# Kernel optimization log

Measured on AMD Instinct MI355X. Metric: run time of the kernel, lower is better.

The kernel has to match this reference:

```python
import jax, jax.numpy as jnp
import numpy as np

N_USERS = 100000
N_ITEMS = 200000
DIM = 64
N_EDGES = 8000000
N_NODES = N_USERS + N_ITEMS


def setup_inputs() -> dict:
    key = jax.random.key(0)
    k1, k2, k3, k4, k5 = jax.random.split(key, 5)
    adj_rows = jax.random.randint(k1, (N_EDGES,), 0, N_NODES, dtype=jnp.int32)
    adj_cols = jax.random.randint(k2, (N_EDGES,), 0, N_NODES, dtype=jnp.int32)
    adj_vals = jax.random.uniform(k3, (N_EDGES,), dtype=jnp.float32)
    # Xavier-uniform style init for embeddings
    bound = float(np.sqrt(6.0 / (N_NODES + DIM)))
    user_emb = jax.random.uniform(k4, (N_USERS, DIM), minval=-bound, maxval=bound, dtype=jnp.float32)
    item_emb = jax.random.uniform(k5, (N_ITEMS, DIM), minval=-bound, maxval=bound, dtype=jnp.float32)
    return {"adj_rows": adj_rows, "adj_cols": adj_cols, "adj_vals": adj_vals,
            "user_emb": user_emb, "item_emb": item_emb}


def reference(adj_rows, adj_cols, adj_vals, user_emb, item_emb):
    n_users = user_emb.shape[0]
    n_nodes = n_users + item_emb.shape[0]
    emb = jnp.concatenate([user_emb, item_emb], axis=0)  # [N, D]
    acc = emb
    cur = emb
    for _ in range(2):  # fixed 2-hop propagation (structural, not data loop)
        # SpMM: cur = A @ cur, A given in COO form
        gathered = cur[adj_cols] * adj_vals[:, None]           # [E, D]
        cur = jax.ops.segment_sum(gathered, adj_rows, num_segments=n_nodes)
        acc = acc + cur
    out = acc / 3.0  # mean over the 3 stacked layer embeddings
    return out[:n_users], out[n_users:]
```

## Files before the change

### kernel.cpp

```cpp
#include <hip/hip_runtime.h>

#define DIM 64
#define PROWS 2048
#define MAXPART 256
#define CHUNK 8192

__device__ __forceinline__ float i2f(int x) { union { int i; float f; } u; u.i = x; return u.f; }
__device__ __forceinline__ float b2f(ushort u) { return __uint_as_float(((unsigned)u) << 16); }
__device__ __forceinline__ ushort f2b(float x) {
    unsigned b = __float_as_uint(x);
    b += 0x7FFFu + ((b >> 16) & 1u);
    return (ushort)(b >> 16);
}
__device__ __forceinline__ unsigned pk(float x, float y) {
    return (unsigned)f2b(x) | ((unsigned)f2b(y) << 16);
}

__global__ __launch_bounds__(256) void k_phist(const int* __restrict__ rows,
                                               int* __restrict__ partCnt,
                                               int nE, int nPart) {
    __shared__ int h[MAXPART];
    for (int t = threadIdx.x; t < nPart; t += 256) h[t] = 0;
    __syncthreads();
    for (long i = (long)blockIdx.x * blockDim.x + threadIdx.x; i < nE;
         i += (long)gridDim.x * blockDim.x)
        atomicAdd(&h[rows[i] >> 11], 1);
    __syncthreads();
    for (int t = threadIdx.x; t < nPart; t += 256) {
        int v = h[t];
        if (v) atomicAdd(&partCnt[t], v);
    }
}

__global__ __launch_bounds__(256) void k_pscan(const int* __restrict__ partCnt,
                                               int* __restrict__ partStart,
                                               int* __restrict__ partCurPad,
                                               int nPart, int nE) {
    __shared__ int s[256];
    const int t = threadIdx.x;
    int v = (t < nPart) ? partCnt[t] : 0;
    s[t] = v; __syncthreads();
    for (int off = 1; off < 256; off <<= 1) {
        int tmp = (t >= off) ? s[t - off] : 0;
        __syncthreads();
        s[t] += tmp;
        __syncthreads();
    }
    if (t < nPart) {
        int excl = s[t] - v;
        partStart[t] = excl;
        partCurPad[t * 16] = excl;
    }
    if (t == 0) partStart[nPart] = nE;
}

__global__ __launch_bounds__(256) void k_scatterP(const int* __restrict__ rows,
                                                  const int* __restrict__ cols,
                                                  const float* __restrict__ vals,
                                                  int* __restrict__ partCurPad,
                                                  int2* __restrict__ pairsA,
                                                  int nE, int nPart) {
    __shared__ int hist[MAXPART];
    __shared__ int runBase[MAXPART];
    const int chunkBase = blockIdx.x * CHUNK;
    int rcache[CHUNK / 256];

    for (int t = threadIdx.x; t < nPart; t += 256) hist[t] = 0;
    __syncthreads();
    #pragma unroll
    for (int j = 0; j < CHUNK / 256; ++j) {
        int i = chunkBase + j * 256 + threadIdx.x;
        int r = (i < nE) ? rows[i] : -1;
        rcache[j] = r;
        if (r >= 0) atomicAdd(&hist[r >> 11], 1);
    }
    __syncthreads();
    for (int t = threadIdx.x; t < nPart; t += 256) {
        int h = hist[t];
        runBase[t] = h ? atomicAdd(&partCurPad[t * 16], h) : 0;
    }
    __syncthreads();
    for (int t = threadIdx.x; t < nPart; t += 256) hist[t] = 0;
    __syncthreads();
    #pragma unroll
    for (int j = 0; j < CHUNK / 256; ++j) {
        int i = chunkBase + j * 256 + threadIdx.x;
        int r = rcache[j];
        if (r >= 0) {
            int p = r >> 11;
            int rank = atomicAdd(&hist[p], 1);
            pairsA[runBase[p] + rank] =
                make_int2(((r & (PROWS - 1)) << 19) | cols[i], __float_as_int(vals[i]));
        }
    }
}

__global__ __launch_bounds__(1024) void k_buildCSR(const int* __restrict__ partStart,
                                                   const int2* __restrict__ pairsA,
                                                   int2* __restrict__ pairsCSR,
                                                   int* __restrict__ rowStart,
                                                   int nNodes, int nE, int nPart) {
    __shared__ int hist[PROWS];
    __shared__ int cur[PROWS];
    __shared__ int s[1024];
    const int p  = blockIdx.x;
    const int r0 = p * PROWS;
    const int segStart = partStart[p], segEnd = partStart[p + 1];
    const int t = threadIdx.x;

    hist[t] = 0; hist[t + 1024] = 0;
    __syncthreads();
    for (int i = segStart + t; i < segEnd; i += 1024)
        atomicAdd(&hist[pairsA[i].x >> 19], 1);
    __syncthreads();

    int a0 = hist[2 * t], a1 = hist[2 * t + 1];
    s[t] = a0 + a1;
    __syncthreads();
    for (int off = 1; off < 1024; off <<= 1) {
        int tmp = (t >= off) ? s[t - off] : 0;
        __syncthreads();
        s[t] += tmp;
        __syncthreads();
    }
    int pairExcl = s[t] - (a0 + a1);
    cur[2 * t]     = segStart + pairExcl;
    cur[2 * t + 1] = segStart + pairExcl + a0;
    __syncthreads();

    int rN = nNodes - r0; if (rN > PROWS) rN = PROWS;
    for (int j = t; j < rN; j += 1024) rowStart[r0 + j] = cur[j];
    if (p == nPart - 1 && t == 0) rowStart[nNodes] = nE;
    __syncthreads();

    for (int i = segStart + t; i < segEnd; i += 1024) {
        int2 e = pairsA[i];
        int lr = e.x >> 19;
        int pos = atomicAdd(&cur[lr], 1);
        pairsCSR[pos] = make_int2(e.x & 0x7FFFF, e.y);
    }
}

__global__ __launch_bounds__(256) void k_toBf16(const float* __restrict__ uE,
                                                const float* __restrict__ iE,
                                                ushort* __restrict__ embB,
                                                int nNodes, int nUsers) {
    const long total8 = (long)nNodes * DIM / 8;
    const long user8  = (long)nUsers * DIM / 8;
    for (long i = (long)blockIdx.x * blockDim.x + threadIdx.x; i < total8;
         i += (long)gridDim.x * blockDim.x) {
        const float4* p = (i < user8) ? (const float4*)uE + 2 * i
                                      : (const float4*)iE + 2 * (i - user8);
        float4 a = p[0], b = p[1];
        uint4 o;
        o.x = pk(a.x, a.y); o.y = pk(a.z, a.w);
        o.z = pk(b.x, b.y); o.w = pk(b.z, b.w);
        ((uint4*)embB)[i] = o;
    }
}

__global__ __launch_bounds__(256) void k_spmm1(const int* __restrict__ rowStart,
                                               const int2* __restrict__ pairs,
                                               const ushort* __restrict__ embB,
                                               ushort* __restrict__ cur1B,
                                               int nNodes) {
    const int lane = threadIdx.x & 63;
    int r = blockIdx.x * (blockDim.x >> 6) + (threadIdx.x >> 6);
    if (r >= nNodes) return;
    int start = __builtin_amdgcn_readfirstlane(rowStart[r]);
    int end   = __builtin_amdgcn_readfirstlane(rowStart[r + 1]);
    float acc = 0.f;
    int e = start;
    for (; e + 7 < end; e += 8) {
        int2 p[8]; float x[8];
        #pragma unroll
        for (int j = 0; j < 8; ++j) p[j] = pairs[e + j];
        #pragma unroll
        for (int j = 0; j < 8; ++j) x[j] = b2f(embB[(size_t)p[j].x * DIM + lane]);
        #pragma unroll
        for (int j = 0; j < 8; ++j) acc = fmaf(i2f(p[j].y), x[j], acc);
    }
    for (; e + 3 < end; e += 4) {
        int2 p[4]; float x[4];
        #pragma unroll
        for (int j = 0; j < 4; ++j) p[j] = pairs[e + j];
        #pragma unroll
        for (int j = 0; j < 4; ++j) x[j] = b2f(embB[(size_t)p[j].x * DIM + lane]);
        #pragma unroll
        for (int j = 0; j < 4; ++j) acc = fmaf(i2f(p[j].y), x[j], acc);
    }
    for (; e < end; ++e) {
        int2 p = pairs[e];
        acc = fmaf(i2f(p.y), b2f(embB[(size_t)p.x * DIM + lane]), acc);
    }
    cur1B[(size_t)r * DIM + lane] = f2b(acc);
}

__global__ __launch_bounds__(256) void k_spmm2(const int* __restrict__ rowStart,
                                               const int2* __restrict__ pairs,
                                               const ushort* __restrict__ cur1B,
                                               const float* __restrict__ uE,
                                               const float* __restrict__ iE,
                                               float* __restrict__ out,
                                               int nNodes, int nUsers) {
    const int lane = threadIdx.x & 63;
    int r = blockIdx.x * (blockDim.x >> 6) + (threadIdx.x >> 6);
    if (r >= nNodes) return;
    int start = __builtin_amdgcn_readfirstlane(rowStart[r]);
    int end   = __builtin_amdgcn_readfirstlane(rowStart[r + 1]);
    float acc = 0.f;
    int e = start;
    for (; e + 7 < end; e += 8) {
        int2 p[8]; float x[8];
        #pragma unroll
        for (int j = 0; j < 8; ++j) p[j] = pairs[e + j];
        #pragma unroll
        for (int j = 0; j < 8; ++j) x[j] = b2f(cur1B[(size_t)p[j].x * DIM + lane]);
        #pragma unroll
        for (int j = 0; j < 8; ++j) acc = fmaf(i2f(p[j].y), x[j], acc);
    }
    for (; e + 3 < end; e += 4) {
        int2 p[4]; float x[4];
        #pragma unroll
        for (int j = 0; j < 4; ++j) p[j] = pairs[e + j];
        #pragma unroll
        for (int j = 0; j < 4; ++j) x[j] = b2f(cur1B[(size_t)p[j].x * DIM + lane]);
        #pragma unroll
        for (int j = 0; j < 4; ++j) acc = fmaf(i2f(p[j].y), x[j], acc);
    }
    for (; e < end; ++e) {
        int2 p = pairs[e];
        acc = fmaf(i2f(p.y), b2f(cur1B[(size_t)p.x * DIM + lane]), acc);
    }
    float em = (r < nUsers) ? uE[(size_t)r * DIM + lane]
                            : iE[(size_t)(r - nUsers) * DIM + lane];
    float c1 = b2f(cur1B[(size_t)r * DIM + lane]);
    float o = (em + c1 + acc) * (1.0f / 3.0f);
    __builtin_nontemporal_store(o, &out[(size_t)r * DIM + lane]);
}

__global__ __launch_bounds__(256) void spmm_scatter(
    const int* __restrict__ rows, const int* __restrict__ cols,
    const float* __restrict__ vals, const float* __restrict__ srcU,
    const float* __restrict__ srcI, float* __restrict__ dst,
    float scale, int nEdges, int nUsers)
{
    const int lane = threadIdx.x & 63;
    const int wavesPerBlock = blockDim.x >> 6;
    long wave = (long)blockIdx.x * wavesPerBlock + (threadIdx.x >> 6);
    const long nWaves = (long)gridDim.x * wavesPerBlock;
    for (long e = wave; e < nEdges; e += nWaves) {
        const int r = rows[e];
        const int c = cols[e];
        const float v = vals[e] * scale;
        const float* src;
        if (srcI != nullptr) {
            src = (c < nUsers) ? (srcU + (size_t)c * DIM)
                               : (srcI + (size_t)(c - nUsers) * DIM);
        } else {
            src = srcU + (size_t)c * DIM;
        }
        atomicAdd(dst + (size_t)r * DIM + lane, v * src[lane]);
    }
}

__global__ __launch_bounds__(256) void finalize_base(
    const float* __restrict__ userE, const float* __restrict__ itemE,
    const float* __restrict__ cur1, float* __restrict__ out, int nNodes, int nUsers)
{
    const long total4 = (long)nNodes * DIM / 4;
    const long user4  = (long)nUsers * DIM / 4;
    const float inv3 = 1.0f / 3.0f;
    for (long i = (long)blockIdx.x * blockDim.x + threadIdx.x; i < total4;
         i += (long)gridDim.x * blockDim.x) {
        float4 e = (i < user4) ? ((const float4*)userE)[i]
                               : ((const float4*)itemE)[i - user4];
        float4 c = ((const float4*)cur1)[i];
        float4 o;
        o.x = (e.x + c.x) * inv3; o.y = (e.y + c.y) * inv3;
        o.z = (e.z + c.z) * inv3; o.w = (e.w + c.w) * inv3;
        ((float4*)out)[i] = o;
    }
}


static inline size_t align256(size_t x) { return (x + 255) & ~(size_t)255; }

extern "C" void kernel_launch(void* const* d_in, const int* in_sizes, int n_in,
                              void* d_out, int out_size, void* d_ws, size_t ws_size,
                              hipStream_t stream)
{
    const int*   rows  = (const int*)d_in[0];
    const int*   cols  = (const int*)d_in[1];
    const float* vals  = (const float*)d_in[2];
    const float* userE = (const float*)d_in[3];
    const float* itemE = (const float*)d_in[4];
    float* out = (float*)d_out;

    const int nE     = in_sizes[0];
    const int nUsers = in_sizes[3] / DIM;
    const int nItems = in_sizes[4] / DIM;
    const int nNodes = nUsers + nItems;
    const int nPart  = (nNodes + PROWS - 1) / PROWS;

    const size_t embBB    = (size_t)nNodes * DIM * sizeof(ushort);
    const size_t cur1BB   = (size_t)nNodes * DIM * sizeof(ushort);
    const size_t cur1F32B = (size_t)nNodes * DIM * sizeof(float);
    const size_t pairsAB  = (size_t)nE * sizeof(int2);
    size_t reg0B = embBB + cur1BB;
    if (pairsAB  > reg0B) reg0B = pairsAB;
    if (cur1F32B > reg0B) reg0B = cur1F32B;
    const size_t csrOff   = align256(reg0B);
    const size_t csrB     = (size_t)nE * sizeof(int2);
    const size_t rsOff    = align256(csrOff + csrB);
    const size_t rsB      = ((size_t)nNodes + 1) * sizeof(int);
    const size_t psOff    = align256(rsOff + rsB);
    const size_t psB      = ((size_t)MAXPART + 1) * sizeof(int);
    const size_t pcOff    = align256(psOff + psB);
    const size_t pcB      = (size_t)MAXPART * 16 * sizeof(int);
    const size_t cntOff   = align256(pcOff + pcB);
    const size_t cntB     = (size_t)MAXPART * sizeof(int);
    const size_t required = cntOff + cntB;

    char* ws = (char*)d_ws;
    int2*   pairsA   = (int2*)ws;
    ushort* embB     = (ushort*)ws;
    ushort* cur1B    = (ushort*)(ws + embBB);
    float*  cur1F32  = (float*)ws;
    int2*   pairsCSR = (int2*)(ws + csrOff);

    if (ws_size >= required && nNodes <= MAXPART * PROWS && nNodes < (1 << 19)) {
        int* rowStart   = (int*)(ws + rsOff);
        int* partStart  = (int*)(ws + psOff);
        int* partCurPad = (int*)(ws + pcOff);
        int* partCnt    = (int*)(ws + cntOff);

        const int nChunks = (nE + CHUNK - 1) / CHUNK;

        hipMemsetAsync(partCnt, 0, (size_t)nPart * sizeof(int), stream);
        k_phist<<<dim3(512), dim3(256), 0, stream>>>(rows, partCnt, nE, nPart);
        k_pscan<<<dim3(1), dim3(256), 0, stream>>>(partCnt, partStart, partCurPad,
                                                   nPart, nE);
        k_scatterP<<<dim3(nChunks), dim3(256), 0, stream>>>(rows, cols, vals,
                                                            partCurPad, pairsA, nE, nPart);
        k_buildCSR<<<dim3(nPart), dim3(1024), 0, stream>>>(partStart, pairsA, pairsCSR,
                                                           rowStart, nNodes, nE, nPart);
        k_toBf16<<<dim3(2048), dim3(256), 0, stream>>>(userE, itemE, embB,
                                                       nNodes, nUsers);

        const int rowsPerBlock = 4;
        dim3 sgrid((nNodes + rowsPerBlock - 1) / rowsPerBlock), sblk(256);
        k_spmm1<<<sgrid, sblk, 0, stream>>>(rowStart, pairsCSR, embB, cur1B, nNodes);
        k_spmm2<<<sgrid, sblk, 0, stream>>>(rowStart, pairsCSR, cur1B, userE, itemE,
                                            out, nNodes, nUsers);
    } else {
        hipMemsetAsync(cur1F32, 0, cur1F32B, stream);
        dim3 blk(256);
        spmm_scatter<<<dim3(4096), blk, 0, stream>>>(rows, cols, vals, userE, itemE,
                                                     cur1F32, 1.0f, nE, nUsers);
        finalize_base<<<dim3(2048), blk, 0, stream>>>(userE, itemE, cur1F32, out,
                                                      nNodes, nUsers);
        spmm_scatter<<<dim3(4096), blk, 0, stream>>>(rows, cols, vals, cur1F32, nullptr,
                                                     out, 1.0f / 3.0f, nE, nUsers);
    }
}
```

Before: 644.7 us.

## Split each CSR row into two column-range segments for gather locality

The CSR build now buckets each row's edges by whether the column index falls in the lower or upper half of the node range, storing two segment offsets per row. The SpMM kernels walk the two segments in order, so all waves tend to touch one half of the embedding table, then the other, with the aim of better L2/MALL locality on the random gathers. In exchange, the shared-memory histogram and scan in buildCSR double in size, the rowStart array doubles, and each row pays extra loop overhead and shorter unrolled runs.

```diff
diff --git a/kernel.cpp b/kernel.cpp
--- a/kernel.cpp
+++ b/kernel.cpp
@@ -4,6 +4,7 @@
 #define PROWS 2048
 #define MAXPART 256
 #define CHUNK 8192
+#define NW 2
 
 __device__ __forceinline__ float i2f(int x) { union { int i; float f; } u; u.i = x; return u.f; }
 __device__ __forceinline__ float b2f(ushort u) { return __uint_as_float(((unsigned)u) << 16); }
@@ -98,24 +99,30 @@
 __global__ __launch_bounds__(1024) void k_buildCSR(const int* __restrict__ partStart,
                                                    const int2* __restrict__ pairsA,
                                                    int2* __restrict__ pairsCSR,
-                                                   int* __restrict__ rowStart,
-                                                   int nNodes, int nE, int nPart) {
-    __shared__ int hist[PROWS];
-    __shared__ int cur[PROWS];
+                                                   int* __restrict__ rowStartW,
+                                                   int nNodes, int nE, int nPart,
+                                                   int split) {
+    __shared__ int hist[PROWS * NW];
+    __shared__ int cur[PROWS * NW];
     __shared__ int s[1024];
     const int p  = blockIdx.x;
     const int r0 = p * PROWS;
     const int segStart = partStart[p], segEnd = partStart[p + 1];
     const int t = threadIdx.x;
 
-    hist[t] = 0; hist[t + 1024] = 0;
-    __syncthreads();
-    for (int i = segStart + t; i < segEnd; i += 1024)
-        atomicAdd(&hist[pairsA[i].x >> 19], 1);
-    __syncthreads();
-
-    int a0 = hist[2 * t], a1 = hist[2 * t + 1];
-    s[t] = a0 + a1;
+    #pragma unroll
+    for (int j = 0; j < NW * 2; ++j) hist[t + j * 1024] = 0;
+    __syncthreads();
+    for (int i = segStart + t; i < segEnd; i += 1024) {
+        int2 e = pairsA[i];
+        int key = ((e.x >> 19) << 1) | (((e.x & 0x7FFFF) >= split) ? 1 : 0);
+        atomicAdd(&hist[key], 1);
+    }
+    __syncthreads();
+
+    int a0 = hist[4 * t], a1 = hist[4 * t + 1], a2 = hist[4 * t + 2], a3 = hist[4 * t + 3];
+    int mySum = a0 + a1 + a2 + a3;
+    s[t] = mySum;
     __syncthreads();
     for (int off = 1; off < 1024; off <<= 1) {
         int tmp = (t >= off) ? s[t - off] : 0;
@@ -123,21 +130,24 @@
         s[t] += tmp;
         __syncthreads();
     }
-    int pairExcl = s[t] - (a0 + a1);
-    cur[2 * t]     = segStart + pairExcl;
-    cur[2 * t + 1] = segStart + pairExcl + a0;
+    int base = segStart + s[t] - mySum;
+    cur[4 * t]     = base;
+    cur[4 * t + 1] = base + a0;
+    cur[4 * t + 2] = base + a0 + a1;
+    cur[4 * t + 3] = base + a0 + a1 + a2;
     __syncthreads();
 
     int rN = nNodes - r0; if (rN > PROWS) rN = PROWS;
-    for (int j = t; j < rN; j += 1024) rowStart[r0 + j] = cur[j];
-    if (p == nPart - 1 && t == 0) rowStart[nNodes] = nE;
+    for (int j = t; j < rN * NW; j += 1024) rowStartW[r0 * NW + j] = cur[j];
+    if (p == nPart - 1 && t == 0) rowStartW[nNodes * NW] = nE;
     __syncthreads();
 
     for (int i = segStart + t; i < segEnd; i += 1024) {
         int2 e = pairsA[i];
-        int lr = e.x >> 19;
-        int pos = atomicAdd(&cur[lr], 1);
-        pairsCSR[pos] = make_int2(e.x & 0x7FFFF, e.y);
+        int c = e.x & 0x7FFFF;
+        int key = ((e.x >> 19) << 1) | ((c >= split) ? 1 : 0);
+        int pos = atomicAdd(&cur[key], 1);
+        pairsCSR[pos] = make_int2(c, e.y);
     }
 }
 
@@ -159,7 +169,7 @@
     }
 }
 
-__global__ __launch_bounds__(256) void k_spmm1(const int* __restrict__ rowStart,
+__global__ __launch_bounds__(256) void k_spmm1(const int* __restrict__ rowStartW,
                                                const int2* __restrict__ pairs,
                                                const ushort* __restrict__ embB,
                                                ushort* __restrict__ cur1B,
@@ -167,36 +177,41 @@
     const int lane = threadIdx.x & 63;
     int r = blockIdx.x * (blockDim.x >> 6) + (threadIdx.x >> 6);
     if (r >= nNodes) return;
-    int start = __builtin_amdgcn_readfirstlane(rowStart[r]);
-    int end   = __builtin_amdgcn_readfirstlane(rowStart[r + 1]);
+    int s0 = __builtin_amdgcn_readfirstlane(rowStartW[r * NW]);
+    int s1 = __builtin_amdgcn_readfirstlane(rowStartW[r * NW + 1]);
+    int s2 = __builtin_amdgcn_readfirstlane(rowStartW[r * NW + 2]);
     float acc = 0.f;
-    int e = start;
-    for (; e + 7 < end; e += 8) {
-        int2 p[8]; float x[8];
-        #pragma unroll
-        for (int j = 0; j < 8; ++j) p[j] = pairs[e + j];
-        #pragma unroll
-        for (int j = 0; j < 8; ++j) x[j] = b2f(embB[(size_t)p[j].x * DIM + lane]);
-        #pragma unroll
-        for (int j = 0; j < 8; ++j) acc = fmaf(i2f(p[j].y), x[j], acc);
-    }
-    for (; e + 3 < end; e += 4) {
-        int2 p[4]; float x[4];
-        #pragma unroll
-        for (int j = 0; j < 4; ++j) p[j] = pairs[e + j];
-        #pragma unroll
-        for (int j = 0; j < 4; ++j) x[j] = b2f(embB[(size_t)p[j].x * DIM + lane]);
-        #pragma unroll
-        for (int j = 0; j < 4; ++j) acc = fmaf(i2f(p[j].y), x[j], acc);
-    }
-    for (; e < end; ++e) {
-        int2 p = pairs[e];
-        acc = fmaf(i2f(p.y), b2f(embB[(size_t)p.x * DIM + lane]), acc);
+    #pragma unroll
+    for (int seg = 0; seg < NW; ++seg) {
+        int e   = (seg == 0) ? s0 : s1;
+        int end = (seg == 0) ? s1 : s2;
+        for (; e + 7 < end; e += 8) {
+            int2 p[8]; float x[8];
+            #pragma unroll
+            for (int j = 0; j < 8; ++j) p[j] = pairs[e + j];
+            #pragma unroll
+            for (int j = 0; j < 8; ++j) x[j] = b2f(embB[(size_t)p[j].x * DIM + lane]);
+            #pragma unroll
+            for (int j = 0; j < 8; ++j) acc = fmaf(i2f(p[j].y), x[j], acc);
+        }
+        for (; e + 3 < end; e += 4) {
+            int2 p[4]; float x[4];
+            #pragma unroll
+            for (int j = 0; j < 4; ++j) p[j] = pairs[e + j];
+            #pragma unroll
+            for (int j = 0; j < 4; ++j) x[j] = b2f(embB[(size_t)p[j].x * DIM + lane]);
+            #pragma unroll
+            for (int j = 0; j < 4; ++j) acc = fmaf(i2f(p[j].y), x[j], acc);
+        }
+        for (; e < end; ++e) {
+            int2 p = pairs[e];
+            acc = fmaf(i2f(p.y), b2f(embB[(size_t)p.x * DIM + lane]), acc);
+        }
     }
     cur1B[(size_t)r * DIM + lane] = f2b(acc);
 }
 
-__global__ __launch_bounds__(256) void k_spmm2(const int* __restrict__ rowStart,
+__global__ __launch_bounds__(256) void k_spmm2(const int* __restrict__ rowStartW,
                                                const int2* __restrict__ pairs,
                                                const ushort* __restrict__ cur1B,
                                                const float* __restrict__ uE,
@@ -206,31 +221,36 @@
     const int lane = threadIdx.x & 63;
     int r = blockIdx.x * (blockDim.x >> 6) + (threadIdx.x >> 6);
     if (r >= nNodes) return;
-    int start = __builtin_amdgcn_readfirstlane(rowStart[r]);
-    int end   = __builtin_amdgcn_readfirstlane(rowStart[r + 1]);
+    int s0 = __builtin_amdgcn_readfirstlane(rowStartW[r * NW]);
+    int s1 = __builtin_amdgcn_readfirstlane(rowStartW[r * NW + 1]);
+    int s2 = __builtin_amdgcn_readfirstlane(rowStartW[r * NW + 2]);
     float acc = 0.f;
-    int e = start;
-    for (; e + 7 < end; e += 8) {
-        int2 p[8]; float x[8];
-        #pragma unroll
-        for (int j = 0; j < 8; ++j) p[j] = pairs[e + j];
-        #pragma unroll
-        for (int j = 0; j < 8; ++j) x[j] = b2f(cur1B[(size_t)p[j].x * DIM + lane]);
-        #pragma unroll
-        for (int j = 0; j < 8; ++j) acc = fmaf(i2f(p[j].y), x[j], acc);
-    }
-    for (; e + 3 < end; e += 4) {
-        int2 p[4]; float x[4];
-        #pragma unroll
-        for (int j = 0; j < 4; ++j) p[j] = pairs[e + j];
-        #pragma unroll
-        for (int j = 0; j < 4; ++j) x[j] = b2f(cur1B[(size_t)p[j].x * DIM + lane]);
-        #pragma unroll
-        for (int j = 0; j < 4; ++j) acc = fmaf(i2f(p[j].y), x[j], acc);
-    }
-    for (; e < end; ++e) {
-        int2 p = pairs[e];
-        acc = fmaf(i2f(p.y), b2f(cur1B[(size_t)p.x * DIM + lane]), acc);
+    #pragma unroll
+    for (int seg = 0; seg < NW; ++seg) {
+        int e   = (seg == 0) ? s0 : s1;
+        int end = (seg == 0) ? s1 : s2;
+        for (; e + 7 < end; e += 8) {
+            int2 p[8]; float x[8];
+            #pragma unroll
+            for (int j = 0; j < 8; ++j) p[j] = pairs[e + j];
+            #pragma unroll
+            for (int j = 0; j < 8; ++j) x[j] = b2f(cur1B[(size_t)p[j].x * DIM + lane]);
+            #pragma unroll
+            for (int j = 0; j < 8; ++j) acc = fmaf(i2f(p[j].y), x[j], acc);
+        }
+        for (; e + 3 < end; e += 4) {
+            int2 p[4]; float x[4];
+            #pragma unroll
+            for (int j = 0; j < 4; ++j) p[j] = pairs[e + j];
+            #pragma unroll
+            for (int j = 0; j < 4; ++j) x[j] = b2f(cur1B[(size_t)p[j].x * DIM + lane]);
+            #pragma unroll
+            for (int j = 0; j < 4; ++j) acc = fmaf(i2f(p[j].y), x[j], acc);
+        }
+        for (; e < end; ++e) {
+            int2 p = pairs[e];
+            acc = fmaf(i2f(p.y), b2f(cur1B[(size_t)p.x * DIM + lane]), acc);
+        }
     }
     float em = (r < nUsers) ? uE[(size_t)r * DIM + lane]
                             : iE[(size_t)(r - nUsers) * DIM + lane];
@@ -302,6 +322,7 @@
     const int nItems = in_sizes[4] / DIM;
     const int nNodes = nUsers + nItems;
     const int nPart  = (nNodes + PROWS - 1) / PROWS;
+    const int split  = nNodes >> 1;
 
     const size_t embBB    = (size_t)nNodes * DIM * sizeof(ushort);
     const size_t cur1BB   = (size_t)nNodes * DIM * sizeof(ushort);
@@ -313,7 +334,7 @@
     const size_t csrOff   = align256(reg0B);
     const size_t csrB     = (size_t)nE * sizeof(int2);
     const size_t rsOff    = align256(csrOff + csrB);
-    const size_t rsB      = ((size_t)nNodes + 1) * sizeof(int);
+    const size_t rsB      = ((size_t)nNodes * NW + 1) * sizeof(int);
     const size_t psOff    = align256(rsOff + rsB);
     const size_t psB      = ((size_t)MAXPART + 1) * sizeof(int);
     const size_t pcOff    = align256(psOff + psB);
@@ -330,7 +351,7 @@
     int2*   pairsCSR = (int2*)(ws + csrOff);
 
     if (ws_size >= required && nNodes <= MAXPART * PROWS && nNodes < (1 << 19)) {
-        int* rowStart   = (int*)(ws + rsOff);
+        int* rowStartW  = (int*)(ws + rsOff);
         int* partStart  = (int*)(ws + psOff);
         int* partCurPad = (int*)(ws + pcOff);
         int* partCnt    = (int*)(ws + cntOff);
@@ -344,14 +365,15 @@
         k_scatterP<<<dim3(nChunks), dim3(256), 0, stream>>>(rows, cols, vals,
                                                             partCurPad, pairsA, nE, nPart);
         k_buildCSR<<<dim3(nPart), dim3(1024), 0, stream>>>(partStart, pairsA, pairsCSR,
-                                                           rowStart, nNodes, nE, nPart);
+                                                           rowStartW, nNodes, nE, nPart,
+                                                           split);
         k_toBf16<<<dim3(2048), dim3(256), 0, stream>>>(userE, itemE, embB,
                                                        nNodes, nUsers);
 
         const int rowsPerBlock = 4;
         dim3 sgrid((nNodes + rowsPerBlock - 1) / rowsPerBlock), sblk(256);
-        k_spmm1<<<sgrid, sblk, 0, stream>>>(rowStart, pairsCSR, embB, cur1B, nNodes);
-        k_spmm2<<<sgrid, sblk, 0, stream>>>(rowStart, pairsCSR, cur1B, userE, itemE,
+        k_spmm1<<<sgrid, sblk, 0, stream>>>(rowStartW, pairsCSR, embB, cur1B, nNodes);
+        k_spmm2<<<sgrid, sblk, 0, stream>>>(rowStartW, pairsCSR, cur1B, userE, itemE,
                                             out, nNodes, nUsers);
     } else {
         hipMemsetAsync(cur1F32, 0, cur1F32B, stream);
```

New measurement: 694.1 us. 7.7% more time.

## Split edge pairs into SoA key/bf16 value arrays and per-wave LDS histograms

Applied to the files above, without the earlier changes.

Edge records change from an int2 (packed key, fp32 value) to separate arrays: a 32-bit key plus a bf16 value, cutting the bytes per edge from 8 to 6 in the scatter, CSR build and both SpMM passes. The histogram and scatter kernels now keep a separate LDS histogram per wavefront to reduce atomic contention, with per-wave write offsets derived from one global atomic per partition. Rounding edge weights to bf16 adds numerical error, and the SoA layout turns one 8-byte load per edge into two narrower loads.

```diff
diff --git a/kernel.cpp b/kernel.cpp
--- a/kernel.cpp
+++ b/kernel.cpp
@@ -5,7 +5,6 @@
 #define MAXPART 256
 #define CHUNK 8192
 
-__device__ __forceinline__ float i2f(int x) { union { int i; float f; } u; u.i = x; return u.f; }
 __device__ __forceinline__ float b2f(ushort u) { return __uint_as_float(((unsigned)u) << 16); }
 __device__ __forceinline__ ushort f2b(float x) {
     unsigned b = __float_as_uint(x);
@@ -19,15 +18,16 @@
 __global__ __launch_bounds__(256) void k_phist(const int* __restrict__ rows,
                                                int* __restrict__ partCnt,
                                                int nE, int nPart) {
-    __shared__ int h[MAXPART];
-    for (int t = threadIdx.x; t < nPart; t += 256) h[t] = 0;
+    __shared__ int h[4][MAXPART];
+    const int wid = threadIdx.x >> 6;
+    for (int t = threadIdx.x; t < 4 * MAXPART; t += 256) h[t >> 8][t & 255] = 0;
     __syncthreads();
     for (long i = (long)blockIdx.x * blockDim.x + threadIdx.x; i < nE;
          i += (long)gridDim.x * blockDim.x)
-        atomicAdd(&h[rows[i] >> 11], 1);
+        atomicAdd(&h[wid][rows[i] >> 11], 1);
     __syncthreads();
     for (int t = threadIdx.x; t < nPart; t += 256) {
-        int v = h[t];
+        int v = h[0][t] + h[1][t] + h[2][t] + h[3][t];
         if (v) atomicAdd(&partCnt[t], v);
     }
 }
@@ -58,29 +58,36 @@
                                                   const int* __restrict__ cols,
                                                   const float* __restrict__ vals,
                                                   int* __restrict__ partCurPad,
-                                                  int2* __restrict__ pairsA,
+                                                  unsigned* __restrict__ keyA,
+                                                  ushort* __restrict__ valA,
                                                   int nE, int nPart) {
-    __shared__ int hist[MAXPART];
-    __shared__ int runBase[MAXPART];
+    __shared__ int hist[4][MAXPART];
+    __shared__ int wOff[4][MAXPART];
     const int chunkBase = blockIdx.x * CHUNK;
+    const int wid = threadIdx.x >> 6;
     int rcache[CHUNK / 256];
 
-    for (int t = threadIdx.x; t < nPart; t += 256) hist[t] = 0;
+    for (int t = threadIdx.x; t < 4 * MAXPART; t += 256) hist[t >> 8][t & 255] = 0;
     __syncthreads();
     #pragma unroll
     for (int j = 0; j < CHUNK / 256; ++j) {
         int i = chunkBase + j * 256 + threadIdx.x;
         int r = (i < nE) ? rows[i] : -1;
         rcache[j] = r;
-        if (r >= 0) atomicAdd(&hist[r >> 11], 1);
+        if (r >= 0) atomicAdd(&hist[wid][r >> 11], 1);
     }
     __syncthreads();
     for (int t = threadIdx.x; t < nPart; t += 256) {
-        int h = hist[t];
-        runBase[t] = h ? atomicAdd(&partCurPad[t * 16], h) : 0;
-    }
-    __syncthreads();
-    for (int t = threadIdx.x; t < nPart; t += 256) hist[t] = 0;
+        int h0 = hist[0][t], h1 = hist[1][t], h2 = hist[2][t], h3 = hist[3][t];
+        int tot = h0 + h1 + h2 + h3;
+        int rb = tot ? atomicAdd(&partCurPad[t * 16], tot) : 0;
+        wOff[0][t] = rb;
+        wOff[1][t] = rb + h0;
+        wOff[2][t] = rb + h0 + h1;
+        wOff[3][t] = rb + h0 + h1 + h2;
+    }
+    __syncthreads();
+    for (int t = threadIdx.x; t < 4 * MAXPART; t += 256) hist[t >> 8][t & 255] = 0;
     __syncthreads();
     #pragma unroll
     for (int j = 0; j < CHUNK / 256; ++j) {
@@ -88,16 +95,19 @@
         int r = rcache[j];
         if (r >= 0) {
             int p = r >> 11;
-            int rank = atomicAdd(&hist[p], 1);
-            pairsA[runBase[p] + rank] =
-                make_int2(((r & (PROWS - 1)) << 19) | cols[i], __float_as_int(vals[i]));
+            int rank = atomicAdd(&hist[wid][p], 1);
+            int pos = wOff[wid][p] + rank;
+            keyA[pos] = (((unsigned)(r & (PROWS - 1))) << 19) | (unsigned)cols[i];
+            valA[pos] = f2b(vals[i]);
         }
     }
 }
 
 __global__ __launch_bounds__(1024) void k_buildCSR(const int* __restrict__ partStart,
-                                                   const int2* __restrict__ pairsA,
-                                                   int2* __restrict__ pairsCSR,
+                                                   const unsigned* __restrict__ keyA,
+                                                   const ushort* __restrict__ valA,
+                                                   unsigned* __restrict__ keyCSR,
+                                                   ushort* __restrict__ valCSR,
                                                    int* __restrict__ rowStart,
                                                    int nNodes, int nE, int nPart) {
     __shared__ int hist[PROWS];
@@ -111,7 +121,7 @@
     hist[t] = 0; hist[t + 1024] = 0;
     __syncthreads();
     for (int i = segStart + t; i < segEnd; i += 1024)
-        atomicAdd(&hist[pairsA[i].x >> 19], 1);
+        atomicAdd(&hist[keyA[i] >> 19], 1);
     __syncthreads();
 
     int a0 = hist[2 * t], a1 = hist[2 * t + 1];
@@ -134,10 +144,11 @@
     __syncthreads();
 
     for (int i = segStart + t; i < segEnd; i += 1024) {
-        int2 e = pairsA[i];
-        int lr = e.x >> 19;
+        unsigned k = keyA[i];
+        int lr = k >> 19;
         int pos = atomicAdd(&cur[lr], 1);
-        pairsCSR[pos] = make_int2(e.x & 0x7FFFF, e.y);
+        keyCSR[pos] = k & 0x7FFFFu;
+        valCSR[pos] = valA[i];
     }
 }
 
@@ -160,7 +171,8 @@
 }
 
 __global__ __launch_bounds__(256) void k_spmm1(const int* __restrict__ rowStart,
-                                               const int2* __restrict__ pairs,
+                                               const unsigned* __restrict__ keys,
+                                               const ushort* __restrict__ vals,
                                                const ushort* __restrict__ embB,
                                                ushort* __restrict__ cur1B,
                                                int nNodes) {
@@ -172,32 +184,31 @@
     float acc = 0.f;
     int e = start;
     for (; e + 7 < end; e += 8) {
-        int2 p[8]; float x[8];
-        #pragma unroll
-        for (int j = 0; j < 8; ++j) p[j] = pairs[e + j];
-        #pragma unroll
-        for (int j = 0; j < 8; ++j) x[j] = b2f(embB[(size_t)p[j].x * DIM + lane]);
-        #pragma unroll
-        for (int j = 0; j < 8; ++j) acc = fmaf(i2f(p[j].y), x[j], acc);
+        unsigned k[8]; float x[8];
+        #pragma unroll
+        for (int j = 0; j < 8; ++j) k[j] = keys[e + j];
+        #pragma unroll
+        for (int j = 0; j < 8; ++j) x[j] = b2f(embB[(size_t)k[j] * DIM + lane]);
+        #pragma unroll
+        for (int j = 0; j < 8; ++j) acc = fmaf(b2f(vals[e + j]), x[j], acc);
     }
     for (; e + 3 < end; e += 4) {
-        int2 p[4]; float x[4];
-        #pragma unroll
-        for (int j = 0; j < 4; ++j) p[j] = pairs[e + j];
-        #pragma unroll
-        for (int j = 0; j < 4; ++j) x[j] = b2f(embB[(size_t)p[j].x * DIM + lane]);
-        #pragma unroll
-        for (int j = 0; j < 4; ++j) acc = fmaf(i2f(p[j].y), x[j], acc);
-    }
-    for (; e < end; ++e) {
-        int2 p = pairs[e];
-        acc = fmaf(i2f(p.y), b2f(embB[(size_t)p.x * DIM + lane]), acc);
-    }
+        unsigned k[4]; float x[4];
+        #pragma unroll
+        for (int j = 0; j < 4; ++j) k[j] = keys[e + j];
+        #pragma unroll
+        for (int j = 0; j < 4; ++j) x[j] = b2f(embB[(size_t)k[j] * DIM + lane]);
+        #pragma unroll
+        for (int j = 0; j < 4; ++j) acc = fmaf(b2f(vals[e + j]), x[j], acc);
+    }
+    for (; e < end; ++e)
+        acc = fmaf(b2f(vals[e]), b2f(embB[(size_t)keys[e] * DIM + lane]), acc);
     cur1B[(size_t)r * DIM + lane] = f2b(acc);
 }
 
 __global__ __launch_bounds__(256) void k_spmm2(const int* __restrict__ rowStart,
-                                               const int2* __restrict__ pairs,
+                                               const unsigned* __restrict__ keys,
+                                               const ushort* __restrict__ vals,
                                                const ushort* __restrict__ cur1B,
                                                const float* __restrict__ uE,
                                                const float* __restrict__ iE,
@@ -211,27 +222,25 @@
     float acc = 0.f;
     int e = start;
     for (; e + 7 < end; e += 8) {
-        int2 p[8]; float x[8];
-        #pragma unroll
-        for (int j = 0; j < 8; ++j) p[j] = pairs[e + j];
-        #pragma unroll
-        for (int j = 0; j < 8; ++j) x[j] = b2f(cur1B[(size_t)p[j].x * DIM + lane]);
-        #pragma unroll
-        for (int j = 0; j < 8; ++j) acc = fmaf(i2f(p[j].y), x[j], acc);
+        unsigned k[8]; float x[8];
+        #pragma unroll
+        for (int j = 0; j < 8; ++j) k[j] = keys[e + j];
+        #pragma unroll
+        for (int j = 0; j < 8; ++j) x[j] = b2f(cur1B[(size_t)k[j] * DIM + lane]);
+        #pragma unroll
+        for (int j = 0; j < 8; ++j) acc = fmaf(b2f(vals[e + j]), x[j], acc);
     }
     for (; e + 3 < end; e += 4) {
-        int2 p[4]; float x[4];
-        #pragma unroll
-        for (int j = 0; j < 4; ++j) p[j] = pairs[e + j];
-        #pragma unroll
-        for (int j = 0; j < 4; ++j) x[j] = b2f(cur1B[(size_t)p[j].x * DIM + lane]);
-        #pragma unroll
-        for (int j = 0; j < 4; ++j) acc = fmaf(i2f(p[j].y), x[j], acc);
-    }
-    for (; e < end; ++e) {
-        int2 p = pairs[e];
-        acc = fmaf(i2f(p.y), b2f(cur1B[(size_t)p.x * DIM + lane]), acc);
-    }
+        unsigned k[4]; float x[4];
+        #pragma unroll
+        for (int j = 0; j < 4; ++j) k[j] = keys[e + j];
+        #pragma unroll
+        for (int j = 0; j < 4; ++j) x[j] = b2f(cur1B[(size_t)k[j] * DIM + lane]);
+        #pragma unroll
+        for (int j = 0; j < 4; ++j) acc = fmaf(b2f(vals[e + j]), x[j], acc);
+    }
+    for (; e < end; ++e)
+        acc = fmaf(b2f(vals[e]), b2f(cur1B[(size_t)keys[e] * DIM + lane]), acc);
     float em = (r < nUsers) ? uE[(size_t)r * DIM + lane]
                             : iE[(size_t)(r - nUsers) * DIM + lane];
     float c1 = b2f(cur1B[(size_t)r * DIM + lane]);
@@ -306,13 +315,17 @@
     const size_t embBB    = (size_t)nNodes * DIM * sizeof(ushort);
     const size_t cur1BB   = (size_t)nNodes * DIM * sizeof(ushort);
     const size_t cur1F32B = (size_t)nNodes * DIM * sizeof(float);
-    const size_t pairsAB  = (size_t)nE * sizeof(int2);
+    const size_t keyAB    = (size_t)nE * sizeof(unsigned);
+    const size_t valAOff  = align256(keyAB);
+    const size_t soaB     = valAOff + (size_t)nE * sizeof(ushort);
     size_t reg0B = embBB + cur1BB;
-    if (pairsAB  > reg0B) reg0B = pairsAB;
+    if (soaB     > reg0B) reg0B = soaB;
     if (cur1F32B > reg0B) reg0B = cur1F32B;
-    const size_t csrOff   = align256(reg0B);
-    const size_t csrB     = (size_t)nE * sizeof(int2);
-    const size_t rsOff    = align256(csrOff + csrB);
+    const size_t kcOff    = align256(reg0B);
+    const size_t kcB      = (size_t)nE * sizeof(unsigned);
+    const size_t vcOff    = align256(kcOff + kcB);
+    const size_t vcB      = (size_t)nE * sizeof(ushort);
+    const size_t rsOff    = align256(vcOff + vcB);
     const size_t rsB      = ((size_t)nNodes + 1) * sizeof(int);
     const size_t psOff    = align256(rsOff + rsB);
     const size_t psB      = ((size_t)MAXPART + 1) * sizeof(int);
@@ -323,11 +336,13 @@
     const size_t required = cntOff + cntB;
 
     char* ws = (char*)d_ws;
-    int2*   pairsA   = (int2*)ws;
-    ushort* embB     = (ushort*)ws;
-    ushort* cur1B    = (ushort*)(ws + embBB);
-    float*  cur1F32  = (float*)ws;
-    int2*   pairsCSR = (int2*)(ws + csrOff);
+    unsigned* keyA    = (unsigned*)ws;
+    ushort*   valA    = (ushort*)(ws + valAOff);
+    ushort*   embB    = (ushort*)ws;
+    ushort*   cur1B   = (ushort*)(ws + embBB);
+    float*    cur1F32 = (float*)ws;
+    unsigned* keyCSR  = (unsigned*)(ws + kcOff);
+    ushort*   valCSR  = (ushort*)(ws + vcOff);
 
     if (ws_size >= required && nNodes <= MAXPART * PROWS && nNodes < (1 << 19)) {
         int* rowStart   = (int*)(ws + rsOff);
@@ -342,17 +357,20 @@
         k_pscan<<<dim3(1), dim3(256), 0, stream>>>(partCnt, partStart, partCurPad,
                                                    nPart, nE);
         k_scatterP<<<dim3(nChunks), dim3(256), 0, stream>>>(rows, cols, vals,
-                                                            partCurPad, pairsA, nE, nPart);
-        k_buildCSR<<<dim3(nPart), dim3(1024), 0, stream>>>(partStart, pairsA, pairsCSR,
-                                                           rowStart, nNodes, nE, nPart);
+                                                            partCurPad, keyA, valA,
+                                                            nE, nPart);
+        k_buildCSR<<<dim3(nPart), dim3(1024), 0, stream>>>(partStart, keyA, valA,
+                                                           keyCSR, valCSR, rowStart,
+                                                           nNodes, nE, nPart);
         k_toBf16<<<dim3(2048), dim3(256), 0, stream>>>(userE, itemE, embB,
                                                        nNodes, nUsers);
 
         const int rowsPerBlock = 4;
         dim3 sgrid((nNodes + rowsPerBlock - 1) / rowsPerBlock), sblk(256);
-        k_spmm1<<<sgrid, sblk, 0, stream>>>(rowStart, pairsCSR, embB, cur1B, nNodes);
-        k_spmm2<<<sgrid, sblk, 0, stream>>>(rowStart, pairsCSR, cur1B, userE, itemE,
-                                            out, nNodes, nUsers);
+        k_spmm1<<<sgrid, sblk, 0, stream>>>(rowStart, keyCSR, valCSR, embB, cur1B,
+                                            nNodes);
+        k_spmm2<<<sgrid, sblk, 0, stream>>>(rowStart, keyCSR, valCSR, cur1B,
+                                            userE, itemE, out, nNodes, nUsers);
     } else {
         hipMemsetAsync(cur1F32, 0, cur1F32B, stream);
         dim3 blk(256);
```

New measurement: 853.0 us. +32.3%, slower.

## Stage partition scatter in LDS and use nontemporal loads for streaming data

Applied to the files above, without the earlier changes.

The partition scatter kernel now sorts each chunk locally in shared memory by partition (local prefix scan plus staging buffer), then writes the staged pairs out so each partition's run is written contiguously. This replaces the direct random global writes with more coalesced ones. Chunk size drops to 4096 so the int2 staging buffer fits in LDS. Separately, streaming reads of rows/cols/vals and the pair arrays in the histogram, CSR build and SpMM kernels become nontemporal loads to reduce cache pollution, which keeps more of the embedding gathers resident in cache.

```diff
diff --git a/kernel.cpp b/kernel.cpp
--- a/kernel.cpp
+++ b/kernel.cpp
@@ -3,7 +3,9 @@
 #define DIM 64
 #define PROWS 2048
 #define MAXPART 256
-#define CHUNK 8192
+#define SCHUNK 4096
+
+typedef int i32x2 __attribute__((ext_vector_type(2)));
 
 __device__ __forceinline__ float i2f(int x) { union { int i; float f; } u; u.i = x; return u.f; }
 __device__ __forceinline__ float b2f(ushort u) { return __uint_as_float(((unsigned)u) << 16); }
@@ -15,6 +17,10 @@
 __device__ __forceinline__ unsigned pk(float x, float y) {
     return (unsigned)f2b(x) | ((unsigned)f2b(y) << 16);
 }
+__device__ __forceinline__ int2 ntload2(const int2* p) {
+    i32x2 v = __builtin_nontemporal_load((const i32x2*)p);
+    return make_int2(v.x, v.y);
+}
 
 __global__ __launch_bounds__(256) void k_phist(const int* __restrict__ rows,
                                                int* __restrict__ partCnt,
@@ -24,7 +30,7 @@
     __syncthreads();
     for (long i = (long)blockIdx.x * blockDim.x + threadIdx.x; i < nE;
          i += (long)gridDim.x * blockDim.x)
-        atomicAdd(&h[rows[i] >> 11], 1);
+        atomicAdd(&h[__builtin_nontemporal_load(&rows[i]) >> 11], 1);
     __syncthreads();
     for (int t = threadIdx.x; t < nPart; t += 256) {
         int v = h[t];
@@ -54,44 +60,68 @@
     if (t == 0) partStart[nPart] = nE;
 }
 
-__global__ __launch_bounds__(256) void k_scatterP(const int* __restrict__ rows,
+__global__ __launch_bounds__(256) void k_scatterS(const int* __restrict__ rows,
                                                   const int* __restrict__ cols,
                                                   const float* __restrict__ vals,
                                                   int* __restrict__ partCurPad,
                                                   int2* __restrict__ pairsA,
                                                   int nE, int nPart) {
     __shared__ int hist[MAXPART];
+    __shared__ int cstart[MAXPART];
     __shared__ int runBase[MAXPART];
-    const int chunkBase = blockIdx.x * CHUNK;
-    int rcache[CHUNK / 256];
-
-    for (int t = threadIdx.x; t < nPart; t += 256) hist[t] = 0;
+    __shared__ int s2[256];
+    __shared__ int2 stage[SCHUNK];
+    __shared__ unsigned char partOf[SCHUNK];
+    const int base = blockIdx.x * SCHUNK;
+    const int cnt  = min(SCHUNK, nE - base);
+    const int t = threadIdx.x;
+    int rc[SCHUNK / 256];
+
+    for (int j = t; j < nPart; j += 256) hist[j] = 0;
     __syncthreads();
     #pragma unroll
-    for (int j = 0; j < CHUNK / 256; ++j) {
-        int i = chunkBase + j * 256 + threadIdx.x;
-        int r = (i < nE) ? rows[i] : -1;
-        rcache[j] = r;
+    for (int j = 0; j < SCHUNK / 256; ++j) {
+        int i = base + j * 256 + t;
+        int r = (i < nE) ? __builtin_nontemporal_load(&rows[i]) : -1;
+        rc[j] = r;
         if (r >= 0) atomicAdd(&hist[r >> 11], 1);
     }
     __syncthreads();
-    for (int t = threadIdx.x; t < nPart; t += 256) {
-        int h = hist[t];
-        runBase[t] = h ? atomicAdd(&partCurPad[t * 16], h) : 0;
-    }
-    __syncthreads();
-    for (int t = threadIdx.x; t < nPart; t += 256) hist[t] = 0;
+    {
+        int v = (t < nPart) ? hist[t] : 0;
+        s2[t] = v; __syncthreads();
+        for (int off = 1; off < 256; off <<= 1) {
+            int tmp = (t >= off) ? s2[t - off] : 0;
+            __syncthreads();
+            s2[t] += tmp;
+            __syncthreads();
+        }
+        if (t < nPart) {
+            cstart[t]  = s2[t] - v;
+            runBase[t] = v ? atomicAdd(&partCurPad[t * 16], v) : 0;
+        }
+    }
+    __syncthreads();
+    for (int j = t; j < nPart; j += 256) hist[j] = 0;
     __syncthreads();
     #pragma unroll
-    for (int j = 0; j < CHUNK / 256; ++j) {
-        int i = chunkBase + j * 256 + threadIdx.x;
-        int r = rcache[j];
+    for (int j = 0; j < SCHUNK / 256; ++j) {
+        int i = base + j * 256 + t;
+        int r = rc[j];
         if (r >= 0) {
             int p = r >> 11;
             int rank = atomicAdd(&hist[p], 1);
-            pairsA[runBase[p] + rank] =
-                make_int2(((r & (PROWS - 1)) << 19) | cols[i], __float_as_int(vals[i]));
+            int slot = cstart[p] + rank;
+            int c = __builtin_nontemporal_load(&cols[i]);
+            float v = __builtin_nontemporal_load(&vals[i]);
+            stage[slot] = make_int2(((r & (PROWS - 1)) << 19) | c, __float_as_int(v));
+            partOf[slot] = (unsigned char)p;
         }
+    }
+    __syncthreads();
+    for (int s = t; s < cnt; s += 256) {
+        int p = partOf[s];
+        pairsA[runBase[p] + (s - cstart[p])] = stage[s];
     }
 }
 
@@ -111,7 +141,7 @@
     hist[t] = 0; hist[t + 1024] = 0;
     __syncthreads();
     for (int i = segStart + t; i < segEnd; i += 1024)
-        atomicAdd(&hist[pairsA[i].x >> 19], 1);
+        atomicAdd(&hist[ntload2(&pairsA[i]).x >> 19], 1);
     __syncthreads();
 
     int a0 = hist[2 * t], a1 = hist[2 * t + 1];
@@ -134,7 +164,7 @@
     __syncthreads();
 
     for (int i = segStart + t; i < segEnd; i += 1024) {
-        int2 e = pairsA[i];
+        int2 e = ntload2(&pairsA[i]);
         int lr = e.x >> 19;
         int pos = atomicAdd(&cur[lr], 1);
         pairsCSR[pos] = make_int2(e.x & 0x7FFFF, e.y);
@@ -174,7 +204,7 @@
     for (; e + 7 < end; e += 8) {
         int2 p[8]; float x[8];
         #pragma unroll
-        for (int j = 0; j < 8; ++j) p[j] = pairs[e + j];
+        for (int j = 0; j < 8; ++j) p[j] = ntload2(&pairs[e + j]);
         #pragma unroll
         for (int j = 0; j < 8; ++j) x[j] = b2f(embB[(size_t)p[j].x * DIM + lane]);
         #pragma unroll
@@ -183,14 +213,14 @@
     for (; e + 3 < end; e += 4) {
         int2 p[4]; float x[4];
         #pragma unroll
-        for (int j = 0; j < 4; ++j) p[j] = pairs[e + j];
+        for (int j = 0; j < 4; ++j) p[j] = ntload2(&pairs[e + j]);
         #pragma unroll
         for (int j = 0; j < 4; ++j) x[j] = b2f(embB[(size_t)p[j].x * DIM + lane]);
         #pragma unroll
         for (int j = 0; j < 4; ++j) acc = fmaf(i2f(p[j].y), x[j], acc);
     }
     for (; e < end; ++e) {
-        int2 p = pairs[e];
+        int2 p = ntload2(&pairs[e]);
         acc = fmaf(i2f(p.y), b2f(embB[(size_t)p.x * DIM + lane]), acc);
     }
     cur1B[(size_t)r * DIM + lane] = f2b(acc);
@@ -213,7 +243,7 @@
     for (; e + 7 < end; e += 8) {
         int2 p[8]; float x[8];
         #pragma unroll
-        for (int j = 0; j < 8; ++j) p[j] = pairs[e + j];
+        for (int j = 0; j < 8; ++j) p[j] = ntload2(&pairs[e + j]);
         #pragma unroll
         for (int j = 0; j < 8; ++j) x[j] = b2f(cur1B[(size_t)p[j].x * DIM + lane]);
         #pragma unroll
@@ -222,14 +252,14 @@
     for (; e + 3 < end; e += 4) {
         int2 p[4]; float x[4];
         #pragma unroll
-        for (int j = 0; j < 4; ++j) p[j] = pairs[e + j];
+        for (int j = 0; j < 4; ++j) p[j] = ntload2(&pairs[e + j]);
         #pragma unroll
         for (int j = 0; j < 4; ++j) x[j] = b2f(cur1B[(size_t)p[j].x * DIM + lane]);
         #pragma unroll
         for (int j = 0; j < 4; ++j) acc = fmaf(i2f(p[j].y), x[j], acc);
     }
     for (; e < end; ++e) {
-        int2 p = pairs[e];
+        int2 p = ntload2(&pairs[e]);
         acc = fmaf(i2f(p.y), b2f(cur1B[(size_t)p.x * DIM + lane]), acc);
     }
     float em = (r < nUsers) ? uE[(size_t)r * DIM + lane]
@@ -335,14 +365,15 @@
         int* partCurPad = (int*)(ws + pcOff);
         int* partCnt    = (int*)(ws + cntOff);
 
-        const int nChunks = (nE + CHUNK - 1) / CHUNK;
+        const int nChunks = (nE + SCHUNK - 1) / SCHUNK;
 
         hipMemsetAsync(partCnt, 0, (size_t)nPart * sizeof(int), stream);
         k_phist<<<dim3(512), dim3(256), 0, stream>>>(rows, partCnt, nE, nPart);
         k_pscan<<<dim3(1), dim3(256), 0, stream>>>(partCnt, partStart, partCurPad,
                                                    nPart, nE);
-        k_scatterP<<<dim3(nChunks), dim3(256), 0, stream>>>(rows, cols, vals,
-                                                            partCurPad, pairsA, nE, nPart);
+        k_scatterS<<<dim3(nChunks), dim3(256), 0, stream>>>(rows, cols, vals,
+                                                            partCurPad, pairsA,
+                                                            nE, nPart);
         k_buildCSR<<<dim3(nPart), dim3(1024), 0, stream>>>(partStart, pairsA, pairsCSR,
                                                            rowStart, nNodes, nE, nPart);
         k_toBf16<<<dim3(2048), dim3(256), 0, stream>>>(userE, itemE, embB,
```

After: 709.8 us. 1.1x slower.
